# Optimization experiments

Measured on AMD Instinct MI355X. Metric: run time of the kernel, lower is better.

Reference implementation:

```python
import jax, jax.numpy as jnp
import numpy as np

N_NODES = 50000
N_EDGES = 800000
D = 128


def setup_inputs() -> dict:
    key = jax.random.key(0)
    ks = jax.random.split(key, 8)
    s = 1.0 / np.sqrt(D)
    return {
        "x": jax.random.normal(ks[0], (N_NODES, D), dtype=jnp.float32),
        "edge_index": jax.random.randint(ks[1], (2, N_EDGES), 0, N_NODES, dtype=jnp.int32),
        "W0l": jax.random.normal(ks[2], (D, D), dtype=jnp.float32) * s,
        "b0l": jnp.zeros((D,), dtype=jnp.float32),
        "W0r": jax.random.normal(ks[3], (D, D), dtype=jnp.float32) * s,
        "W1l": jax.random.normal(ks[4], (D, D), dtype=jnp.float32) * s,
        "b1l": jnp.zeros((D,), dtype=jnp.float32),
        "W1r": jax.random.normal(ks[5], (D, D), dtype=jnp.float32) * s,
    }


def reference(x, edge_index, W0l, b0l, W0r, W1l, b1l, W1r):
    # Encoder(conv='sage', num_layers=2), eval mode (dropout = identity).
    src = edge_index[0]  # x_j gathered from source nodes
    dst = edge_index[1]  # aggregated at target nodes
    # in-degree for mean aggregation; isolated nodes get 0 aggregate (PyG mean)
    deg = jax.ops.segment_sum(jnp.ones_like(dst, dtype=x.dtype), dst, num_segments=N_NODES)
    inv_deg = jnp.where(deg > 0, 1.0 / jnp.maximum(deg, 1.0), 0.0)[:, None]

    def sage(h, Wl, bl, Wr):
        m = h @ Wl + bl                                        # lin_l
        agg = jax.ops.segment_sum(m[src], dst, num_segments=N_NODES) * inv_deg  # mean aggr
        return agg + h @ Wr                                    # + lin_r skip

    h = jax.nn.relu(sage(x, W0l, b0l, W0r))   # layer 0 + relu
    return sage(h, W1l, b1l, W1r)             # final layer
```

## Files before the change

kernel.cpp:

```cpp
#include <hip/hip_runtime.h>

#define N_NODES 50000
#define N_EDGES 800000
#define D 128
#define NBLK ((N_NODES + 255) / 256)
#define EPB 4096
#define CAP 8192

typedef __bf16 bf16x8 __attribute__((ext_vector_type(8)));
typedef short s16x8 __attribute__((ext_vector_type(8)));
typedef float f32x4 __attribute__((ext_vector_type(4)));
typedef unsigned short u16;
typedef unsigned int u32;
typedef u32 u32x4 __attribute__((ext_vector_type(4)));

__device__ inline u16 f32_to_bf16(float f) {
    u32 u = __builtin_bit_cast(u32, f);
    u += 0x7fffu + ((u >> 16) & 1u);
    return (u16)(u >> 16);
}
__device__ inline float bf16_lo(u32 v) { return __builtin_bit_cast(float, v << 16); }
__device__ inline float bf16_hi(u32 v) { return __builtin_bit_cast(float, v & 0xffff0000u); }

__device__ inline f32x4 mfma16(s16x8 a, s16x8 b, f32x4 c) {
    return __builtin_amdgcn_mfma_f32_16x16x32_bf16(
        __builtin_bit_cast(bf16x8, a), __builtin_bit_cast(bf16x8, b), c, 0, 0, 0);
}

#define CAST_BLOCKS ((N_NODES * 16) / 256)
#define STAGE_BLOCKS ((N_EDGES + EPB - 1) / EPB)

__global__ __launch_bounds__(256) void prep_stage(
    const float* __restrict__ x, u16* __restrict__ xb,
    const float* __restrict__ W0l, const float* __restrict__ W0r,
    const float* __restrict__ W1l, const float* __restrict__ W1r,
    u16* __restrict__ Wp,
    const int* __restrict__ src, const int* __restrict__ dst,
    int* __restrict__ ccount, u32* __restrict__ staged) {
    __shared__ int hist[NBLK];
    __shared__ int base[NBLK];
    int t = threadIdx.x, b = blockIdx.x;
    if (b < CAST_BLOCKS) {
        int gid = b * 256 + t;
        const float* p = x + (size_t)gid * 8;
        f32x4 a = *(const f32x4*)p;
        f32x4 c = *(const f32x4*)(p + 4);
        u16 o[8];
#pragma unroll
        for (int j = 0; j < 4; j++) { o[j] = f32_to_bf16(a[j]); o[4 + j] = f32_to_bf16(c[j]); }
        *(s16x8*)(xb + (size_t)gid * 8) = *(const s16x8*)o;
    } else if (b < CAST_BLOCKS + 32) {
        int gid = (b - CAST_BLOCKS) * 256 + t;
        int wsel = gid >> 11;
        int rem  = gid & 2047;
        int ct   = rem >> 8;
        int ks   = (rem >> 6) & 3;
        int lane = rem & 63;
        const float* W = (wsel == 0) ? W0l : (wsel == 1) ? W0r : (wsel == 2) ? W1l : W1r;
        int n  = ct * 16 + (lane & 15);
        int k0 = ks * 32 + (lane >> 4) * 8;
        u16 o[8];
#pragma unroll
        for (int j = 0; j < 8; j++) o[j] = f32_to_bf16(W[(k0 + j) * D + n]);
        u16* dp = Wp + wsel * 16384 + (size_t)((ct * 4 + ks) * 64 + lane) * 8;
        *(s16x8*)dp = *(const s16x8*)o;
    } else {
        int sb = b - CAST_BLOCKS - 32;
        int bb = sb * EPB;
        if (t < NBLK) hist[t] = 0;
        __syncthreads();
        u32 pk[16]; int cb[16];
#pragma unroll
        for (int i = 0; i < 16; i++) {
            int e = bb + i * 256 + t;
            if (e < N_EDGES) {
                int sv = src[e], dv = dst[e];
                pk[i] = (u32)sv | ((u32)(dv & 255) << 16);
                cb[i] = dv >> 8;
                atomicAdd(&hist[cb[i]], 1);
            } else cb[i] = -1;
        }
        __syncthreads();
        if (t < NBLK) {
            int c = hist[t];
            if (c > 0) {
                int old = atomicAdd(&ccount[t], c);
                if (old > CAP - c) old = CAP - c;
                base[t] = t * CAP + old;
            }
            hist[t] = 0;
        }
        __syncthreads();
#pragma unroll
        for (int i = 0; i < 16; i++) {
            if (cb[i] >= 0) {
                int slot = atomicAdd(&hist[cb[i]], 1);
                staged[base[cb[i]] + slot] = pk[i];
            }
        }
    }
}

__global__ __launch_bounds__(256) void fine_kernel(const int* __restrict__ ccount,
                                                   const u32* __restrict__ staged,
                                                   u16* __restrict__ eidx,
                                                   int* __restrict__ rowptr,
                                                   float* __restrict__ inv) {
    __shared__ u32 sdata[CAP];
    __shared__ int hist[256];
    __shared__ int cursor[256];
    __shared__ int sc[256];
    __shared__ int wsum[4];
    int t = threadIdx.x, cb = blockIdx.x;
    int lane = t & 63, wave = t >> 6;

    int cc = (t < NBLK) ? ccount[t] : 0;
    int cv = cc > CAP ? CAP : cc;
    int s = cv;
#pragma unroll
    for (int off = 1; off < 64; off <<= 1) {
        int u = __shfl_up(s, off, 64);
        if (lane >= off) s += u;
    }
    if (lane == 63) wsum[wave] = s;
    hist[t] = 0;
    __syncthreads();
    int wadd = 0;
#pragma unroll
    for (int w = 0; w < 4; w++) if (w < wave) wadd += wsum[w];
    sc[t] = s - cv + wadd;
    __syncthreads();
    int gbase = sc[cb];
    int c = ccount[cb];
    if (c > CAP) c = CAP;

    for (int i = t; i < c; i += 256) {
        u32 v = staged[cb * CAP + i];
        sdata[i] = v;
        atomicAdd(&hist[(v >> 16) & 255], 1);
    }
    __syncthreads();
    int d = hist[t];
    s = d;
#pragma unroll
    for (int off = 1; off < 64; off <<= 1) {
        int u = __shfl_up(s, off, 64);
        if (lane >= off) s += u;
    }
    if (lane == 63) wsum[wave] = s;
    __syncthreads();
    wadd = 0;
#pragma unroll
    for (int w = 0; w < 4; w++) if (w < wave) wadd += wsum[w];
    int excl = gbase + s - d + wadd;
    int node = cb * 256 + t;
    if (node < N_NODES) {
        rowptr[node] = excl;
        inv[node] = d > 0 ? 1.0f / (float)d : 0.0f;
    }
    cursor[t] = excl;
    if (cb == 0 && t == 0) rowptr[N_NODES] = N_EDGES;
    __syncthreads();
    for (int i = t; i < c; i += 256) {
        u32 v = sdata[i];
        int pos = atomicAdd(&cursor[(v >> 16) & 255], 1);
        eidx[pos] = (u16)(v & 0xffffu);
    }
}

template <int RELU, int OUTF32>
__global__ __launch_bounds__(256) void fused_layer(
    const u16* __restrict__ A,
    const u16* __restrict__ WpR, const u16* __restrict__ WpL,
    const float* __restrict__ bias, const float* __restrict__ inv,
    const int* __restrict__ rowptr, const u16* __restrict__ eidx,
    u16* __restrict__ outb, float* __restrict__ outf) {
    __shared__ char mlds[16 * 256];
    int wave = threadIdx.x >> 6, lane = threadIdx.x & 63;
    int rowbase = blockIdx.x * 16;
    int quad = lane >> 4, ql = lane & 15;

#pragma unroll 1
    for (int i = 0; i < 4; i++) {
        int node = rowbase + wave * 4 + i;
        int start = rowptr[node], end = rowptr[node + 1];
        float a0=0.f,a1=0.f,a2=0.f,a3=0.f,a4=0.f,a5=0.f,a6=0.f,a7=0.f;
        int base = start;
        for (; base + 16 <= end; base += 16) {
            int i0 = base + quad;
            int s0 = eidx[i0], s1 = eidx[i0 + 4], s2 = eidx[i0 + 8], s3 = eidx[i0 + 12];
            u32x4 v0 = *(const u32x4*)(A + (size_t)s0 * D + ql * 8);
            u32x4 v1 = *(const u32x4*)(A + (size_t)s1 * D + ql * 8);
            u32x4 v2 = *(const u32x4*)(A + (size_t)s2 * D + ql * 8);
            u32x4 v3 = *(const u32x4*)(A + (size_t)s3 * D + ql * 8);
            a0 += bf16_lo(v0.x) + bf16_lo(v1.x) + bf16_lo(v2.x) + bf16_lo(v3.x);
            a1 += bf16_hi(v0.x) + bf16_hi(v1.x) + bf16_hi(v2.x) + bf16_hi(v3.x);
            a2 += bf16_lo(v0.y) + bf16_lo(v1.y) + bf16_lo(v2.y) + bf16_lo(v3.y);
            a3 += bf16_hi(v0.y) + bf16_hi(v1.y) + bf16_hi(v2.y) + bf16_hi(v3.y);
            a4 += bf16_lo(v0.z) + bf16_lo(v1.z) + bf16_lo(v2.z) + bf16_lo(v3.z);
            a5 += bf16_hi(v0.z) + bf16_hi(v1.z) + bf16_hi(v2.z) + bf16_hi(v3.z);
            a6 += bf16_lo(v0.w) + bf16_lo(v1.w) + bf16_lo(v2.w) + bf16_lo(v3.w);
            a7 += bf16_hi(v0.w) + bf16_hi(v1.w) + bf16_hi(v2.w) + bf16_hi(v3.w);
        }
        for (; base < end; base += 4) {
            int ii = base + quad;
            if (ii < end) {
                u32x4 v = *(const u32x4*)(A + (size_t)eidx[ii] * D + ql * 8);
                a0 += bf16_lo(v.x); a1 += bf16_hi(v.x);
                a2 += bf16_lo(v.y); a3 += bf16_hi(v.y);
                a4 += bf16_lo(v.z); a5 += bf16_hi(v.z);
                a6 += bf16_lo(v.w); a7 += bf16_hi(v.w);
            }
        }
        a0 += __shfl_xor(a0, 16); a0 += __shfl_xor(a0, 32);
        a1 += __shfl_xor(a1, 16); a1 += __shfl_xor(a1, 32);
        a2 += __shfl_xor(a2, 16); a2 += __shfl_xor(a2, 32);
        a3 += __shfl_xor(a3, 16); a3 += __shfl_xor(a3, 32);
        a4 += __shfl_xor(a4, 16); a4 += __shfl_xor(a4, 32);
        a5 += __shfl_xor(a5, 16); a5 += __shfl_xor(a5, 32);
        a6 += __shfl_xor(a6, 16); a6 += __shfl_xor(a6, 32);
        a7 += __shfl_xor(a7, 16); a7 += __shfl_xor(a7, 32);
        if (quad == 0) {
            float iv = inv[node];
            u32x4 o;
            o.x = (u32)f32_to_bf16(a0 * iv) | ((u32)f32_to_bf16(a1 * iv) << 16);
            o.y = (u32)f32_to_bf16(a2 * iv) | ((u32)f32_to_bf16(a3 * iv) << 16);
            o.z = (u32)f32_to_bf16(a4 * iv) | ((u32)f32_to_bf16(a5 * iv) << 16);
            o.w = (u32)f32_to_bf16(a6 * iv) | ((u32)f32_to_bf16(a7 * iv) << 16);
            int lr = wave * 4 + i;
            *(u32x4*)(mlds + lr * 256 + ((ql ^ lr) & 15) * 16) = o;
        }
    }

    s16x8 bR[2][4], bL[2][4];
#pragma unroll
    for (int ct = 0; ct < 2; ct++) {
        int ctg = wave * 2 + ct;
#pragma unroll
        for (int ks = 0; ks < 4; ks++) {
            size_t off = (size_t)((ctg * 4 + ks) * 64 + lane) * 8;
            bR[ct][ks] = *(const s16x8*)(WpR + off);
            bL[ct][ks] = *(const s16x8*)(WpL + off);
        }
    }
    __syncthreads();

    f32x4 acc[2];
    acc[0] = (f32x4){0.f, 0.f, 0.f, 0.f};
    acc[1] = (f32x4){0.f, 0.f, 0.f, 0.f};
#pragma unroll
    for (int ks = 0; ks < 4; ks++) {
        s16x8 a1 = *(const s16x8*)(A + (size_t)(rowbase + ql) * D + ks * 32 + quad * 8);
        s16x8 a2 = *(const s16x8*)(mlds + ql * 256 + (((ks * 4 + quad) ^ ql) & 15) * 16);
#pragma unroll
        for (int ct = 0; ct < 2; ct++) {
            acc[ct] = mfma16(a1, bR[ct][ks], acc[ct]);
            acc[ct] = mfma16(a2, bL[ct][ks], acc[ct]);
        }
    }

    float bv[2];
#pragma unroll
    for (int ct = 0; ct < 2; ct++) bv[ct] = bias[wave * 32 + ct * 16 + ql];

#pragma unroll
    for (int i = 0; i < 4; i++) {
        int row = rowbase + quad * 4 + i;
        float mask = inv[row] > 0.f ? 1.f : 0.f;
#pragma unroll
        for (int ct = 0; ct < 2; ct++) {
            int col = wave * 32 + ct * 16 + ql;
            float v = acc[ct][i] + mask * bv[ct];
            if (RELU) v = v > 0.f ? v : 0.f;
            if (OUTF32) outf[(size_t)row * D + col] = v;
            else        outb[(size_t)row * D + col] = f32_to_bf16(v);
        }
    }
}

extern "C" void kernel_launch(void* const* d_in, const int* in_sizes, int n_in,
                              void* d_out, int out_size, void* d_ws, size_t ws_size,
                              hipStream_t stream) {
    const float* x    = (const float*)d_in[0];
    const int*   edge = (const int*)d_in[1];
    const int*   src  = edge;
    const int*   dstn = edge + N_EDGES;
    const float* W0l  = (const float*)d_in[2];
    const float* b0l  = (const float*)d_in[3];
    const float* W0r  = (const float*)d_in[4];
    const float* W1l  = (const float*)d_in[5];
    const float* b1l  = (const float*)d_in[6];
    const float* W1r  = (const float*)d_in[7];
    float* out = (float*)d_out;

    char* p = (char*)d_ws;
    auto alloc = [&](size_t nb) { char* r = p; p += (nb + 255) & ~(size_t)255; return r; };
    int*   ccount = (int*)alloc((size_t)NBLK * 4);
    int*   rowptr = (int*)alloc((size_t)(N_NODES + 1) * 4);
    float* inv    = (float*)alloc((size_t)N_NODES * 4);
    u32*   staged = (u32*)alloc((size_t)NBLK * CAP * 4);
    u16*   eidx   = (u16*)alloc((size_t)N_EDGES * 2);
    u16*   xb     = (u16*)alloc((size_t)N_NODES * D * 2);
    u16*   hb     = (u16*)alloc((size_t)N_NODES * D * 2);
    u16*   Wp     = (u16*)alloc((size_t)4 * 16384 * 2);

    hipMemsetAsync(ccount, 0, (size_t)NBLK * 4, stream);

    prep_stage<<<CAST_BLOCKS + 32 + STAGE_BLOCKS, 256, 0, stream>>>(
        x, xb, W0l, W0r, W1l, W1r, Wp, src, dstn, ccount, staged);
    fine_kernel<<<NBLK, 256, 0, stream>>>(ccount, staged, eidx, rowptr, inv);

    int fblocks = N_NODES / 16;
    const u16* WpL0 = Wp;
    const u16* WpR0 = Wp + 16384;
    const u16* WpL1 = Wp + 2 * 16384;
    const u16* WpR1 = Wp + 3 * 16384;
    fused_layer<1, 0><<<fblocks, 256, 0, stream>>>(xb, WpR0, WpL0, b0l, inv, rowptr, eidx, hb, nullptr);
    fused_layer<0, 1><<<fblocks, 256, 0, stream>>>(hb, WpR1, WpL1, b1l, inv, rowptr, eidx, nullptr, out);
}
```

Before: 218.9 us.

## Pad CSR rows to 16 with dummy zero row and interleave four-row gathers

Each node's neighbor list is padded to a multiple of 16 using a sentinel index that points to an all-zero extra row appended to the feature buffers. Row start and round count are packed into one info word per node, which removes the global prefix scan and the tail loop. The gather loop now walks four nodes at once, issuing up to 16 independent row loads per round to raise memory-level parallelism. The cost is extra padded loads, more registers for accumulators, and a per-bucket capacity limit (PCAP) on padded edges.

```diff
diff --git a/kernel.cpp b/kernel.cpp
--- a/kernel.cpp
+++ b/kernel.cpp
@@ -6,6 +6,7 @@
 #define NBLK ((N_NODES + 255) / 256)
 #define EPB 4096
 #define CAP 8192
+#define PCAP 8192
 
 typedef __bf16 bf16x8 __attribute__((ext_vector_type(8)));
 typedef short s16x8 __attribute__((ext_vector_type(8)));
@@ -31,7 +32,7 @@
 #define STAGE_BLOCKS ((N_EDGES + EPB - 1) / EPB)
 
 __global__ __launch_bounds__(256) void prep_stage(
-    const float* __restrict__ x, u16* __restrict__ xb,
+    const float* __restrict__ x, u16* __restrict__ xb, u16* __restrict__ hb,
     const float* __restrict__ W0l, const float* __restrict__ W0r,
     const float* __restrict__ W1l, const float* __restrict__ W1r,
     u16* __restrict__ Wp,
@@ -64,8 +65,11 @@
         for (int j = 0; j < 8; j++) o[j] = f32_to_bf16(W[(k0 + j) * D + n]);
         u16* dp = Wp + wsel * 16384 + (size_t)((ct * 4 + ks) * 64 + lane) * 8;
         *(s16x8*)dp = *(const s16x8*)o;
+    } else if (b < CAST_BLOCKS + 33) {
+        if (t < 64)       ((u32*)(xb + (size_t)N_NODES * D))[t] = 0;
+        else if (t < 128) ((u32*)(hb + (size_t)N_NODES * D))[t - 64] = 0;
     } else {
-        int sb = b - CAST_BLOCKS - 32;
+        int sb = b - CAST_BLOCKS - 33;
         int bb = sb * EPB;
         if (t < NBLK) hist[t] = 0;
         __syncthreads();
@@ -104,36 +108,19 @@
 __global__ __launch_bounds__(256) void fine_kernel(const int* __restrict__ ccount,
                                                    const u32* __restrict__ staged,
                                                    u16* __restrict__ eidx,
-                                                   int* __restrict__ rowptr,
+                                                   u32* __restrict__ info,
                                                    float* __restrict__ inv) {
     __shared__ u32 sdata[CAP];
     __shared__ int hist[256];
     __shared__ int cursor[256];
-    __shared__ int sc[256];
     __shared__ int wsum[4];
     int t = threadIdx.x, cb = blockIdx.x;
     int lane = t & 63, wave = t >> 6;
 
-    int cc = (t < NBLK) ? ccount[t] : 0;
-    int cv = cc > CAP ? CAP : cc;
-    int s = cv;
-#pragma unroll
-    for (int off = 1; off < 64; off <<= 1) {
-        int u = __shfl_up(s, off, 64);
-        if (lane >= off) s += u;
-    }
-    if (lane == 63) wsum[wave] = s;
     hist[t] = 0;
     __syncthreads();
-    int wadd = 0;
-#pragma unroll
-    for (int w = 0; w < 4; w++) if (w < wave) wadd += wsum[w];
-    sc[t] = s - cv + wadd;
-    __syncthreads();
-    int gbase = sc[cb];
     int c = ccount[cb];
     if (c > CAP) c = CAP;
-
     for (int i = t; i < c; i += 256) {
         u32 v = staged[cb * CAP + i];
         sdata[i] = v;
@@ -141,7 +128,8 @@
     }
     __syncthreads();
     int d = hist[t];
-    s = d;
+    int pd = (d + 15) & ~15;
+    int s = pd;
 #pragma unroll
     for (int off = 1; off < 64; off <<= 1) {
         int u = __shfl_up(s, off, 64);
@@ -149,23 +137,23 @@
     }
     if (lane == 63) wsum[wave] = s;
     __syncthreads();
-    wadd = 0;
+    int wadd = 0;
 #pragma unroll
     for (int w = 0; w < 4; w++) if (w < wave) wadd += wsum[w];
-    int excl = gbase + s - d + wadd;
+    int gb = cb * PCAP + (s - pd + wadd);
     int node = cb * 256 + t;
     if (node < N_NODES) {
-        rowptr[node] = excl;
+        info[node] = (u32)gb | ((u32)(pd >> 4) << 21);
         inv[node] = d > 0 ? 1.0f / (float)d : 0.0f;
     }
-    cursor[t] = excl;
-    if (cb == 0 && t == 0) rowptr[N_NODES] = N_EDGES;
+    cursor[t] = gb;
     __syncthreads();
     for (int i = t; i < c; i += 256) {
         u32 v = sdata[i];
         int pos = atomicAdd(&cursor[(v >> 16) & 255], 1);
         eidx[pos] = (u16)(v & 0xffffu);
     }
+    for (int i = gb + d; i < gb + pd; i++) eidx[i] = (u16)N_NODES;
 }
 
 template <int RELU, int OUTF32>
@@ -173,61 +161,75 @@
     const u16* __restrict__ A,
     const u16* __restrict__ WpR, const u16* __restrict__ WpL,
     const float* __restrict__ bias, const float* __restrict__ inv,
-    const int* __restrict__ rowptr, const u16* __restrict__ eidx,
+    const u32* __restrict__ info, const u16* __restrict__ eidx,
     u16* __restrict__ outb, float* __restrict__ outf) {
     __shared__ char mlds[16 * 256];
     int wave = threadIdx.x >> 6, lane = threadIdx.x & 63;
     int rowbase = blockIdx.x * 16;
     int quad = lane >> 4, ql = lane & 15;
 
+    int basek[4], rnds[4];
+#pragma unroll
+    for (int k = 0; k < 4; k++) {
+        u32 ifo = info[rowbase + wave * 4 + k];
+        basek[k] = (int)(ifo & 0x1FFFFFu);
+        rnds[k]  = (int)(ifo >> 21);
+    }
+    int maxr = rnds[0];
+#pragma unroll
+    for (int k = 1; k < 4; k++) maxr = rnds[k] > maxr ? rnds[k] : maxr;
+
+    float acc[4][8];
+#pragma unroll
+    for (int k = 0; k < 4; k++)
+#pragma unroll
+        for (int j = 0; j < 8; j++) acc[k][j] = 0.f;
+
 #pragma unroll 1
-    for (int i = 0; i < 4; i++) {
-        int node = rowbase + wave * 4 + i;
-        int start = rowptr[node], end = rowptr[node + 1];
-        float a0=0.f,a1=0.f,a2=0.f,a3=0.f,a4=0.f,a5=0.f,a6=0.f,a7=0.f;
-        int base = start;
-        for (; base + 16 <= end; base += 16) {
-            int i0 = base + quad;
-            int s0 = eidx[i0], s1 = eidx[i0 + 4], s2 = eidx[i0 + 8], s3 = eidx[i0 + 12];
-            u32x4 v0 = *(const u32x4*)(A + (size_t)s0 * D + ql * 8);
-            u32x4 v1 = *(const u32x4*)(A + (size_t)s1 * D + ql * 8);
-            u32x4 v2 = *(const u32x4*)(A + (size_t)s2 * D + ql * 8);
-            u32x4 v3 = *(const u32x4*)(A + (size_t)s3 * D + ql * 8);
-            a0 += bf16_lo(v0.x) + bf16_lo(v1.x) + bf16_lo(v2.x) + bf16_lo(v3.x);
-            a1 += bf16_hi(v0.x) + bf16_hi(v1.x) + bf16_hi(v2.x) + bf16_hi(v3.x);
-            a2 += bf16_lo(v0.y) + bf16_lo(v1.y) + bf16_lo(v2.y) + bf16_lo(v3.y);
-            a3 += bf16_hi(v0.y) + bf16_hi(v1.y) + bf16_hi(v2.y) + bf16_hi(v3.y);
-            a4 += bf16_lo(v0.z) + bf16_lo(v1.z) + bf16_lo(v2.z) + bf16_lo(v3.z);
-            a5 += bf16_hi(v0.z) + bf16_hi(v1.z) + bf16_hi(v2.z) + bf16_hi(v3.z);
-            a6 += bf16_lo(v0.w) + bf16_lo(v1.w) + bf16_lo(v2.w) + bf16_lo(v3.w);
-            a7 += bf16_hi(v0.w) + bf16_hi(v1.w) + bf16_hi(v2.w) + bf16_hi(v3.w);
-        }
-        for (; base < end; base += 4) {
-            int ii = base + quad;
-            if (ii < end) {
-                u32x4 v = *(const u32x4*)(A + (size_t)eidx[ii] * D + ql * 8);
-                a0 += bf16_lo(v.x); a1 += bf16_hi(v.x);
-                a2 += bf16_lo(v.y); a3 += bf16_hi(v.y);
-                a4 += bf16_lo(v.z); a5 += bf16_hi(v.z);
-                a6 += bf16_lo(v.w); a7 += bf16_hi(v.w);
+    for (int r = 0; r < maxr; r++) {
+        u32x4 g[4][4];
+#pragma unroll
+        for (int k = 0; k < 4; k++) {
+            if (r < rnds[k]) {
+                int i0 = basek[k] + r * 16 + quad;
+                int s0 = eidx[i0], s1 = eidx[i0 + 4], s2 = eidx[i0 + 8], s3 = eidx[i0 + 12];
+                g[k][0] = *(const u32x4*)(A + (size_t)s0 * D + ql * 8);
+                g[k][1] = *(const u32x4*)(A + (size_t)s1 * D + ql * 8);
+                g[k][2] = *(const u32x4*)(A + (size_t)s2 * D + ql * 8);
+                g[k][3] = *(const u32x4*)(A + (size_t)s3 * D + ql * 8);
             }
         }
-        a0 += __shfl_xor(a0, 16); a0 += __shfl_xor(a0, 32);
-        a1 += __shfl_xor(a1, 16); a1 += __shfl_xor(a1, 32);
-        a2 += __shfl_xor(a2, 16); a2 += __shfl_xor(a2, 32);
-        a3 += __shfl_xor(a3, 16); a3 += __shfl_xor(a3, 32);
-        a4 += __shfl_xor(a4, 16); a4 += __shfl_xor(a4, 32);
-        a5 += __shfl_xor(a5, 16); a5 += __shfl_xor(a5, 32);
-        a6 += __shfl_xor(a6, 16); a6 += __shfl_xor(a6, 32);
-        a7 += __shfl_xor(a7, 16); a7 += __shfl_xor(a7, 32);
+#pragma unroll
+        for (int k = 0; k < 4; k++) {
+            if (r < rnds[k]) {
+#pragma unroll
+                for (int j = 0; j < 4; j++) {
+                    u32x4 v = g[k][j];
+                    acc[k][0] += bf16_lo(v.x); acc[k][1] += bf16_hi(v.x);
+                    acc[k][2] += bf16_lo(v.y); acc[k][3] += bf16_hi(v.y);
+                    acc[k][4] += bf16_lo(v.z); acc[k][5] += bf16_hi(v.z);
+                    acc[k][6] += bf16_lo(v.w); acc[k][7] += bf16_hi(v.w);
+                }
+            }
+        }
+    }
+
+#pragma unroll
+    for (int k = 0; k < 4; k++) {
+#pragma unroll
+        for (int j = 0; j < 8; j++) {
+            acc[k][j] += __shfl_xor(acc[k][j], 16);
+            acc[k][j] += __shfl_xor(acc[k][j], 32);
+        }
         if (quad == 0) {
+            int node = rowbase + wave * 4 + k;
             float iv = inv[node];
             u32x4 o;
-            o.x = (u32)f32_to_bf16(a0 * iv) | ((u32)f32_to_bf16(a1 * iv) << 16);
-            o.y = (u32)f32_to_bf16(a2 * iv) | ((u32)f32_to_bf16(a3 * iv) << 16);
-            o.z = (u32)f32_to_bf16(a4 * iv) | ((u32)f32_to_bf16(a5 * iv) << 16);
-            o.w = (u32)f32_to_bf16(a6 * iv) | ((u32)f32_to_bf16(a7 * iv) << 16);
-            int lr = wave * 4 + i;
+            o.x = (u32)f32_to_bf16(acc[k][0] * iv) | ((u32)f32_to_bf16(acc[k][1] * iv) << 16);
+            o.y = (u32)f32_to_bf16(acc[k][2] * iv) | ((u32)f32_to_bf16(acc[k][3] * iv) << 16);
+            o.z = (u32)f32_to_bf16(acc[k][4] * iv) | ((u32)f32_to_bf16(acc[k][5] * iv) << 16);
+            o.w = (u32)f32_to_bf16(acc[k][6] * iv) | ((u32)f32_to_bf16(acc[k][7] * iv) << 16);
+            int lr = wave * 4 + k;
             *(u32x4*)(mlds + lr * 256 + ((ql ^ lr) & 15) * 16) = o;
         }
     }
@@ -245,17 +247,17 @@
     }
     __syncthreads();
 
-    f32x4 acc[2];
-    acc[0] = (f32x4){0.f, 0.f, 0.f, 0.f};
-    acc[1] = (f32x4){0.f, 0.f, 0.f, 0.f};
+    f32x4 acc2[2];
+    acc2[0] = (f32x4){0.f, 0.f, 0.f, 0.f};
+    acc2[1] = (f32x4){0.f, 0.f, 0.f, 0.f};
 #pragma unroll
     for (int ks = 0; ks < 4; ks++) {
         s16x8 a1 = *(const s16x8*)(A + (size_t)(rowbase + ql) * D + ks * 32 + quad * 8);
         s16x8 a2 = *(const s16x8*)(mlds + ql * 256 + (((ks * 4 + quad) ^ ql) & 15) * 16);
 #pragma unroll
         for (int ct = 0; ct < 2; ct++) {
-            acc[ct] = mfma16(a1, bR[ct][ks], acc[ct]);
-            acc[ct] = mfma16(a2, bL[ct][ks], acc[ct]);
+            acc2[ct] = mfma16(a1, bR[ct][ks], acc2[ct]);
+            acc2[ct] = mfma16(a2, bL[ct][ks], acc2[ct]);
         }
     }
 
@@ -270,7 +272,7 @@
 #pragma unroll
         for (int ct = 0; ct < 2; ct++) {
             int col = wave * 32 + ct * 16 + ql;
-            float v = acc[ct][i] + mask * bv[ct];
+            float v = acc2[ct][i] + mask * bv[ct];
             if (RELU) v = v > 0.f ? v : 0.f;
             if (OUTF32) outf[(size_t)row * D + col] = v;
             else        outb[(size_t)row * D + col] = f32_to_bf16(v);
@@ -296,25 +298,25 @@
     char* p = (char*)d_ws;
     auto alloc = [&](size_t nb) { char* r = p; p += (nb + 255) & ~(size_t)255; return r; };
     int*   ccount = (int*)alloc((size_t)NBLK * 4);
-    int*   rowptr = (int*)alloc((size_t)(N_NODES + 1) * 4);
+    u32*   info   = (u32*)alloc((size_t)N_NODES * 4);
     float* inv    = (float*)alloc((size_t)N_NODES * 4);
     u32*   staged = (u32*)alloc((size_t)NBLK * CAP * 4);
-    u16*   eidx   = (u16*)alloc((size_t)N_EDGES * 2);
-    u16*   xb     = (u16*)alloc((size_t)N_NODES * D * 2);
-    u16*   hb     = (u16*)alloc((size_t)N_NODES * D * 2);
+    u16*   eidx   = (u16*)alloc((size_t)NBLK * PCAP * 2);
+    u16*   xb     = (u16*)alloc((size_t)(N_NODES + 1) * D * 2);
+    u16*   hb     = (u16*)alloc((size_t)(N_NODES + 1) * D * 2);
     u16*   Wp     = (u16*)alloc((size_t)4 * 16384 * 2);
 
     hipMemsetAsync(ccount, 0, (size_t)NBLK * 4, stream);
 
-    prep_stage<<<CAST_BLOCKS + 32 + STAGE_BLOCKS, 256, 0, stream>>>(
-        x, xb, W0l, W0r, W1l, W1r, Wp, src, dstn, ccount, staged);
-    fine_kernel<<<NBLK, 256, 0, stream>>>(ccount, staged, eidx, rowptr, inv);
+    prep_stage<<<CAST_BLOCKS + 33 + STAGE_BLOCKS, 256, 0, stream>>>(
+        x, xb, hb, W0l, W0r, W1l, W1r, Wp, src, dstn, ccount, staged);
+    fine_kernel<<<NBLK, 256, 0, stream>>>(ccount, staged, eidx, info, inv);
 
     int fblocks = N_NODES / 16;
     const u16* WpL0 = Wp;
     const u16* WpR0 = Wp + 16384;
     const u16* WpL1 = Wp + 2 * 16384;
     const u16* WpR1 = Wp + 3 * 16384;
-    fused_layer<1, 0><<<fblocks, 256, 0, stream>>>(xb, WpR0, WpL0, b0l, inv, rowptr, eidx, hb, nullptr);
-    fused_layer<0, 1><<<fblocks, 256, 0, stream>>>(hb, WpR1, WpL1, b1l, inv, rowptr, eidx, nullptr, out);
-}
+    fused_layer<1, 0><<<fblocks, 256, 0, stream>>>(xb, WpR0, WpL0, b0l, inv, info, eidx, hb, nullptr);
+    fused_layer<0, 1><<<fblocks, 256, 0, stream>>>(hb, WpR1, WpL1, b1l, inv, info, eidx, nullptr, out);
+}
```

After: 219.0 us. About the same (+0.1%).
